# Kernel optimization log

Hardware: AMD Instinct MI355X
Metric: run time of the kernel (lower is better)

## Reference

```python
import jax, jax.numpy as jnp
import numpy as np

N_NODES = 50000


def _gcn_norm(edge_index, num_nodes):
    """PyG GCNConv normalization: add self-loops, symmetric deg^{-1/2} weights."""
    loops = jnp.arange(num_nodes, dtype=edge_index.dtype)
    src = jnp.concatenate([edge_index[0], loops])
    dst = jnp.concatenate([edge_index[1], loops])
    deg = jax.ops.segment_sum(jnp.ones_like(dst, dtype=jnp.float32), dst,
                              num_segments=num_nodes)
    dinv = jax.lax.rsqrt(jnp.maximum(deg, 1.0))  # self-loops guarantee deg>=1
    norm = dinv[src] * dinv[dst]                 # [E + N]
    return src, dst, norm


def _gcn_conv(x, W, b, src, dst, norm, num_nodes):
    h = x @ W                                    # [N, out] dense GEMM
    msg = h[src] * norm[:, None]                 # gather + scale
    agg = jax.ops.segment_sum(msg, dst, num_segments=num_nodes)
    return agg + b


def setup_inputs() -> dict:
    key = jax.random.key(0)
    ks = jax.random.split(key, 8)
    d = 128
    scale = 1.0 / np.sqrt(d)
    emb = jax.random.normal(ks[0], (N_NODES, d), dtype=jnp.float32)
    W1 = jax.random.normal(ks[1], (d, d), dtype=jnp.float32) * scale
    W2 = jax.random.normal(ks[2], (d, d), dtype=jnp.float32) * scale
    W3 = jax.random.normal(ks[3], (d, d), dtype=jnp.float32) * scale
    b1 = jnp.zeros((d,), dtype=jnp.float32)
    b2 = jnp.zeros((d,), dtype=jnp.float32)
    b3 = jnp.zeros((d,), dtype=jnp.float32)
    edge_index = jax.random.randint(ks[4], (2, 600000), 0, N_NODES, dtype=jnp.int64)
    return {"emb": emb, "W1": W1, "b1": b1, "W2": W2, "b2": b2,
            "W3": W3, "b3": b3, "edge_index": edge_index}


def reference(emb, W1, b1, W2, b2, W3, b3, edge_index):
    # Eval-mode forward: F.dropout(training=False) is identity.
    src, dst, norm = _gcn_norm(edge_index, N_NODES)
    x = emb
    x = jax.nn.relu(_gcn_conv(x, W1, b1, src, dst, norm, N_NODES))
    x = jax.nn.relu(_gcn_conv(x, W2, b2, src, dst, norm, N_NODES))
    x = _gcn_conv(x, W3, b3, src, dst, norm, N_NODES)
    x = x.at[0].set(0.0)  # x[0] = zeros(x.shape[1])
    return x
```

## Files before the change

### kernel.cpp

```cpp
#include <hip/hip_runtime.h>
#include <hip/hip_fp16.h>

#define NN 50000
#define D 128
#define STRIDE 64

typedef __attribute__((ext_vector_type(16))) float f32x16;
typedef _Float16 h16;
typedef __attribute__((ext_vector_type(8))) _Float16 h16x8;

struct alignas(16) H8 { h16 h[8]; };

typedef const __attribute__((address_space(1))) void gvoid;
typedef __attribute__((address_space(3))) void lvoid;

__global__ __launch_bounds__(256) void wprep_kernel(const float* __restrict__ W1,
                                                    const float* __restrict__ W2,
                                                    const float* __restrict__ W3,
                                                    h16* __restrict__ Wsp,
                                                    int* __restrict__ cnt) {
    const int b  = blockIdx.x;
    const int w  = b >> 3;
    const int ks = b & 7;
    const float* W = w == 0 ? W1 : (w == 1 ? W2 : W3);
    h16* dst = Wsp + w * 32768;
    const int l  = threadIdx.x & 63;
    const int ct = threadIdx.x >> 6;
    const int n  = ct * 32 + (l & 31);
    const int lh = l >> 5;
    const int kbase = ks * 16 + lh * 8;
    H8 hi8, lo8;
#pragma unroll
    for (int j = 0; j < 8; j++) {
        float wv = W[(kbase + j) * D + n];
        h16 hi = (h16)wv;
        hi8.h[j] = hi;
        lo8.h[j] = (h16)(wv - (float)hi);
    }
    const int base = ((ks * 4 + ct) * 64 + l) * 8;
    *(H8*)(dst + base)         = hi8;
    *(H8*)(dst + base + 16384) = lo8;
    for (int i = b * 256 + threadIdx.x; i < NN; i += 24 * 256) cnt[i] = 0;
}

__global__ __launch_bounds__(512, 4) void gemm_mfma(const void* __restrict__ Xv, int x_is_f32,
                                                    const h16* __restrict__ Wsp,
                                                    h16* __restrict__ H, int M,
                                                    const int* __restrict__ srcA,
                                                    const int* __restrict__ dstA,
                                                    int* __restrict__ cnt,
                                                    int* __restrict__ slots, int noct) {
    __shared__ h16 Ws[32768];
    {
        const int t = threadIdx.x;
#pragma unroll
        for (int i = 0; i < 8; i++) {
            const int off = (i * 512 + t) * 8;
            __builtin_amdgcn_global_load_lds((gvoid*)(Wsp + off), (lvoid*)(Ws + off),
                                             16, 0, 0);
        }
    }
    __syncthreads();

    const int wave = threadIdx.x >> 6;
    const int lane = threadIdx.x & 63;
    const int row0 = blockIdx.x * 256 + wave * 32;
    const int arow = min(row0 + (lane & 31), M - 1);
    const int koff = (lane >> 5) * 8;

    f32x16 acc[4] = {};

#pragma unroll
    for (int ks = 0; ks < 8; ks++) {
        h16x8 ahi, alo;
        if (x_is_f32) {
            const float* p = (const float*)Xv + (size_t)arow * D + koff + ks * 16;
            float4 fa = *(const float4*)p;
            float4 fb = *(const float4*)(p + 4);
            float f[8] = {fa.x, fa.y, fa.z, fa.w, fb.x, fb.y, fb.z, fb.w};
#pragma unroll
            for (int j = 0; j < 8; j++) {
                h16 hi = (h16)f[j];
                ahi[j] = hi;
                alo[j] = (h16)(f[j] - (float)hi);
            }
        } else {
            const h16* p = (const h16*)Xv + (size_t)arow * D + koff + ks * 16;
            ahi = *(const h16x8*)p;
        }
#pragma unroll
        for (int ct = 0; ct < 4; ct++) {
            const int base = ((ks * 4 + ct) * 64 + lane) * 8;
            h16x8 bhi = *(const h16x8*)(Ws + base);
            h16x8 blo = *(const h16x8*)(Ws + base + 16384);
            acc[ct] = __builtin_amdgcn_mfma_f32_32x32x16_f16(ahi, bhi, acc[ct], 0, 0, 0);
            acc[ct] = __builtin_amdgcn_mfma_f32_32x32x16_f16(ahi, blo, acc[ct], 0, 0, 0);
            if (x_is_f32)
                acc[ct] = __builtin_amdgcn_mfma_f32_32x32x16_f16(alo, bhi, acc[ct], 0, 0, 0);
        }
    }

    __syncthreads();
    {
        h16* C_lds = Ws;
        const int col0 = lane & 31;
        const int lr0  = 4 * (lane >> 5);
#pragma unroll
        for (int ct = 0; ct < 4; ct++) {
#pragma unroll
            for (int r = 0; r < 16; r++) {
                const int lrow = lr0 + (r & 3) + 8 * (r >> 2);
                C_lds[(wave * 32 + lrow) * D + ct * 32 + col0] = (h16)acc[ct][r];
            }
        }
        const h16* src = C_lds + wave * 32 * D;
        h16* gdst = H + (size_t)row0 * D;
#pragma unroll
        for (int j = 0; j < 8; j++) {
            const int i = j * 64 + lane;
            const int row = row0 + (i >> 4);
            if (row < M)
                *(h16x8*)(gdst + (size_t)i * 8) = *(const h16x8*)(src + i * 8);
        }
    }

    if (srcA) {
        int t = blockIdx.x * 512 + threadIdx.x;
        if (t < noct) {
            int4 sa = ((const int4*)srcA)[2 * t];
            int4 sb = ((const int4*)srcA)[2 * t + 1];
            int4 da = ((const int4*)dstA)[2 * t];
            int4 db = ((const int4*)dstA)[2 * t + 1];
            int p0 = atomicAdd(&cnt[da.x], 1);
            int p1 = atomicAdd(&cnt[da.y], 1);
            int p2 = atomicAdd(&cnt[da.z], 1);
            int p3 = atomicAdd(&cnt[da.w], 1);
            int p4 = atomicAdd(&cnt[db.x], 1);
            int p5 = atomicAdd(&cnt[db.y], 1);
            int p6 = atomicAdd(&cnt[db.z], 1);
            int p7 = atomicAdd(&cnt[db.w], 1);
            if (p0 < STRIDE - 4) slots[da.x * STRIDE + p0] = sa.x;
            if (p1 < STRIDE - 4) slots[da.y * STRIDE + p1] = sa.y;
            if (p2 < STRIDE - 4) slots[da.z * STRIDE + p2] = sa.z;
            if (p3 < STRIDE - 4) slots[da.w * STRIDE + p3] = sa.w;
            if (p4 < STRIDE - 4) slots[db.x * STRIDE + p4] = sb.x;
            if (p5 < STRIDE - 4) slots[db.y * STRIDE + p5] = sb.y;
            if (p6 < STRIDE - 4) slots[db.z * STRIDE + p6] = sb.z;
            if (p7 < STRIDE - 4) slots[db.w * STRIDE + p7] = sb.w;
        }
    }
}

__global__ __launch_bounds__(256) void agg_kernel(const h16* __restrict__ H,
                                                  const int* __restrict__ cnt,
                                                  const int* __restrict__ slots,
                                                  const float* __restrict__ bias,
                                                  h16* __restrict__ out16,
                                                  float* __restrict__ out32,
                                                  int mode) {
    const int lane  = threadIdx.x & 63;
    const int q     = lane >> 4;
    const int col   = (lane & 15) * 8;
    const int node0 = blockIdx.x * 16 + (threadIdx.x >> 6) * 4;

    const float4 bb0 = *(const float4*)(bias + col);
    const float4 bb1 = *(const float4*)(bias + col + 4);

    int cA[4], sa0[4], sb0[4];
#pragma unroll
    for (int nn = 0; nn < 4; nn++) {
        cA[nn]  = cnt[node0 + nn];
        sa0[nn] = slots[(node0 + nn) * STRIDE + q];
        sb0[nn] = slots[(node0 + nn) * STRIDE + 4 + q];
    }

#pragma unroll 1
    for (int nn = 0; nn < 4; nn++) {
        const int node = node0 + nn;
        const int c = __builtin_amdgcn_readfirstlane(cA[nn]);
        const float di = rsqrtf((float)c + 1.0f);
        const int sbase = node * STRIDE;
        const int pc = min((c + 8) & ~7, STRIDE);

        float aA[8] = {0.f, 0.f, 0.f, 0.f, 0.f, 0.f, 0.f, 0.f};
        float aB[8] = {0.f, 0.f, 0.f, 0.f, 0.f, 0.f, 0.f, 0.f};

        int sa = sa0[nn];
        int sb = sb0[nn];

        for (int p = 0; p < pc; p += 8) {
            int sa_n = slots[sbase + min(p + 8 + q, STRIDE - 1)];
            int sb_n = slots[sbase + min(p + 12 + q, STRIDE - 1)];
            const int ja = p + q;
            const int jb = p + 4 + q;
            const int ca = (ja < c) ? sa : node;
            const int cb = (jb < c) ? sb : node;
            float wa = (ja < c) ? rsqrtf((float)cnt[ca] + 1.0f) : ((ja == c) ? di : 0.f);
            float wb = (jb < c) ? rsqrtf((float)cnt[cb] + 1.0f) : ((jb == c) ? di : 0.f);
            h16x8 va = *(const h16x8*)(H + (size_t)ca * D + col);
            h16x8 vb = *(const h16x8*)(H + (size_t)cb * D + col);
#pragma unroll
            for (int j = 0; j < 8; j++) {
                aA[j] = fmaf(wa, (float)va[j], aA[j]);
                aB[j] = fmaf(wb, (float)vb[j], aB[j]);
            }
            sa = sa_n; sb = sb_n;
        }

#pragma unroll
        for (int j = 0; j < 8; j++) {
            float v = aA[j] + aB[j];
            v += __shfl_xor(v, 16, 64);
            v += __shfl_xor(v, 32, 64);
            aA[j] = v;
        }

        if (lane < 16) {
            float r[8];
            r[0] = fmaf(di, aA[0], bb0.x); r[1] = fmaf(di, aA[1], bb0.y);
            r[2] = fmaf(di, aA[2], bb0.z); r[3] = fmaf(di, aA[3], bb0.w);
            r[4] = fmaf(di, aA[4], bb1.x); r[5] = fmaf(di, aA[5], bb1.y);
            r[6] = fmaf(di, aA[6], bb1.z); r[7] = fmaf(di, aA[7], bb1.w);
            if (mode == 0) {
                h16x8 o;
#pragma unroll
                for (int j = 0; j < 8; j++) o[j] = (h16)fmaxf(r[j], 0.f);
                *(h16x8*)(out16 + (size_t)node * D + col) = o;
            } else {
                if (node == 0) {
#pragma unroll
                    for (int j = 0; j < 8; j++) r[j] = 0.f;
                }
                *(float4*)(out32 + (size_t)node * D + col)     = make_float4(r[0], r[1], r[2], r[3]);
                *(float4*)(out32 + (size_t)node * D + col + 4) = make_float4(r[4], r[5], r[6], r[7]);
            }
        }
    }
}


extern "C" void kernel_launch(void* const* d_in, const int* in_sizes, int n_in,
                              void* d_out, int out_size, void* d_ws, size_t ws_size,
                              hipStream_t stream) {
    const float* emb = (const float*)d_in[0];
    const float* W1  = (const float*)d_in[1];
    const float* b1  = (const float*)d_in[2];
    const float* W2  = (const float*)d_in[3];
    const float* b2  = (const float*)d_in[4];
    const float* W3  = (const float*)d_in[5];
    const float* b3  = (const float*)d_in[6];
    const int*   ei  = (const int*)d_in[7];

    const int E = in_sizes[7] / 2;
    const int* srcA = ei;
    const int* dstA = ei + E;
    float* out = (float*)d_out;

    char* ws = (char*)d_ws;
    size_t off = 0;
    auto alloc = [&](size_t bytes) -> void* {
        void* p = ws + off;
        off = (off + bytes + 255) & ~(size_t)255;
        return p;
    };
    h16* h      = (h16*)alloc((size_t)NN * D * 2);
    h16* x16    = (h16*)alloc((size_t)NN * D * 2);
    int* cnt    = (int*)alloc((size_t)NN * 4);
    int* slots  = (int*)alloc((size_t)NN * STRIDE * 4);
    h16* Wsp    = (h16*)alloc((size_t)3 * 32768 * 2);

    const int gemm_grid = (NN + 255) / 256;
    const int agg_grid  = NN / 16;
    const int noct = E / 8;

    wprep_kernel<<<24, 256, 0, stream>>>(W1, W2, W3, Wsp, cnt);
    gemm_mfma<<<gemm_grid, 512, 0, stream>>>(emb, 1, Wsp, h, NN,
                                             srcA, dstA, cnt, slots, noct);
    agg_kernel<<<agg_grid, 256, 0, stream>>>(h, cnt, slots, b1, x16, nullptr, 0);
    gemm_mfma<<<gemm_grid, 512, 0, stream>>>(x16, 0, Wsp + 32768, h, NN,
                                             nullptr, nullptr, nullptr, nullptr, 0);
    agg_kernel<<<agg_grid, 256, 0, stream>>>(h, cnt, slots, b2, x16, nullptr, 0);
    gemm_mfma<<<gemm_grid, 512, 0, stream>>>(x16, 0, Wsp + 65536, h, NN,
                                             nullptr, nullptr, nullptr, nullptr, 0);
    agg_kernel<<<agg_grid, 256, 0, stream>>>(h, cnt, slots, b3, nullptr, out, 1);
}
```

Before: 244.0 us.

## Fuse aggregation with next layer GEMM using 16x16 MFMA tiles

Layers 1 and 2 now run a single fused kernel. Each wave aggregates 16 nodes into LDS, applies bias and relu, then multiplies the tile by the next weight matrix using 16x16x32 MFMA with hi/lo weight splitting. This removes the separate GEMM launches and the global round-trip of the intermediate activations. The weight prep emits a new fragment layout for W2 and W3, and the edge loads in the first GEMM are hoisted before the barrier. The trade-off is that each fused wave reads weights from global or L2 rather than LDS, and aggregation occupancy may change.

```diff
diff --git a/kernel.cpp b/kernel.cpp
--- a/kernel.cpp
+++ b/kernel.cpp
@@ -6,6 +6,7 @@
 #define STRIDE 64
 
 typedef __attribute__((ext_vector_type(16))) float f32x16;
+typedef __attribute__((ext_vector_type(4)))  float f32x4;
 typedef _Float16 h16;
 typedef __attribute__((ext_vector_type(8))) _Float16 h16x8;
 
@@ -21,29 +22,47 @@
                                                     int* __restrict__ cnt) {
     const int b  = blockIdx.x;
     const int w  = b >> 3;
-    const int ks = b & 7;
     const float* W = w == 0 ? W1 : (w == 1 ? W2 : W3);
     h16* dst = Wsp + w * 32768;
     const int l  = threadIdx.x & 63;
     const int ct = threadIdx.x >> 6;
-    const int n  = ct * 32 + (l & 31);
-    const int lh = l >> 5;
-    const int kbase = ks * 16 + lh * 8;
-    H8 hi8, lo8;
-#pragma unroll
-    for (int j = 0; j < 8; j++) {
-        float wv = W[(kbase + j) * D + n];
-        h16 hi = (h16)wv;
-        hi8.h[j] = hi;
-        lo8.h[j] = (h16)(wv - (float)hi);
-    }
-    const int base = ((ks * 4 + ct) * 64 + l) * 8;
-    *(H8*)(dst + base)         = hi8;
-    *(H8*)(dst + base + 16384) = lo8;
+
+    if (w == 0) {
+        const int ks = b & 7;
+        const int n  = ct * 32 + (l & 31);
+        const int kbase = ks * 16 + (l >> 5) * 8;
+        H8 hi8, lo8;
+#pragma unroll
+        for (int j = 0; j < 8; j++) {
+            float wv = W[(kbase + j) * D + n];
+            h16 hi = (h16)wv;
+            hi8.h[j] = hi;
+            lo8.h[j] = (h16)(wv - (float)hi);
+        }
+        const int base = ((ks * 4 + ct) * 64 + l) * 8;
+        *(H8*)(dst + base)         = hi8;
+        *(H8*)(dst + base + 16384) = lo8;
+    } else {
+        const int f  = (b & 7) * 4 + ct;
+        const int ks = f >> 3, nt = f & 7;
+        const int kbase = ks * 32 + (l >> 4) * 8;
+        const int n = nt * 16 + (l & 15);
+        H8 hi8, lo8;
+#pragma unroll
+        for (int j = 0; j < 8; j++) {
+            float wv = W[(kbase + j) * D + n];
+            h16 hi = (h16)wv;
+            hi8.h[j] = hi;
+            lo8.h[j] = (h16)(wv - (float)hi);
+        }
+        const int base = (f * 64 + l) * 8;
+        *(H8*)(dst + base)         = hi8;
+        *(H8*)(dst + base + 16384) = lo8;
+    }
     for (int i = b * 256 + threadIdx.x; i < NN; i += 24 * 256) cnt[i] = 0;
 }
 
-__global__ __launch_bounds__(512, 4) void gemm_mfma(const void* __restrict__ Xv, int x_is_f32,
+__global__ __launch_bounds__(512, 4) void gemm_mfma(const void* __restrict__ Xv,
                                                     const h16* __restrict__ Wsp,
                                                     h16* __restrict__ H, int M,
                                                     const int* __restrict__ srcA,
@@ -60,6 +79,20 @@
                                              16, 0, 0);
         }
     }
+
+    int4 esa, esb, eda, edb;
+    bool do_fill = false;
+    {
+        int t = blockIdx.x * 512 + threadIdx.x;
+        if (t < noct) {
+            do_fill = true;
+            esa = ((const int4*)srcA)[2 * t];
+            esb = ((const int4*)srcA)[2 * t + 1];
+            eda = ((const int4*)dstA)[2 * t];
+            edb = ((const int4*)dstA)[2 * t + 1];
+        }
+    }
+
     __syncthreads();
 
     const int wave = threadIdx.x >> 6;
@@ -73,20 +106,15 @@
 #pragma unroll
     for (int ks = 0; ks < 8; ks++) {
         h16x8 ahi, alo;
-        if (x_is_f32) {
-            const float* p = (const float*)Xv + (size_t)arow * D + koff + ks * 16;
-            float4 fa = *(const float4*)p;
-            float4 fb = *(const float4*)(p + 4);
-            float f[8] = {fa.x, fa.y, fa.z, fa.w, fb.x, fb.y, fb.z, fb.w};
-#pragma unroll
-            for (int j = 0; j < 8; j++) {
-                h16 hi = (h16)f[j];
-                ahi[j] = hi;
-                alo[j] = (h16)(f[j] - (float)hi);
-            }
-        } else {
-            const h16* p = (const h16*)Xv + (size_t)arow * D + koff + ks * 16;
-            ahi = *(const h16x8*)p;
+        const float* p = (const float*)Xv + (size_t)arow * D + koff + ks * 16;
+        float4 fa = *(const float4*)p;
+        float4 fb = *(const float4*)(p + 4);
+        float f[8] = {fa.x, fa.y, fa.z, fa.w, fb.x, fb.y, fb.z, fb.w};
+#pragma unroll
+        for (int j = 0; j < 8; j++) {
+            h16 hi = (h16)f[j];
+            ahi[j] = hi;
+            alo[j] = (h16)(f[j] - (float)hi);
         }
 #pragma unroll
         for (int ct = 0; ct < 4; ct++) {
@@ -95,8 +123,7 @@
             h16x8 blo = *(const h16x8*)(Ws + base + 16384);
             acc[ct] = __builtin_amdgcn_mfma_f32_32x32x16_f16(ahi, bhi, acc[ct], 0, 0, 0);
             acc[ct] = __builtin_amdgcn_mfma_f32_32x32x16_f16(ahi, blo, acc[ct], 0, 0, 0);
-            if (x_is_f32)
-                acc[ct] = __builtin_amdgcn_mfma_f32_32x32x16_f16(alo, bhi, acc[ct], 0, 0, 0);
+            acc[ct] = __builtin_amdgcn_mfma_f32_32x32x16_f16(alo, bhi, acc[ct], 0, 0, 0);
         }
     }
 
@@ -124,29 +151,143 @@
         }
     }
 
-    if (srcA) {
-        int t = blockIdx.x * 512 + threadIdx.x;
-        if (t < noct) {
-            int4 sa = ((const int4*)srcA)[2 * t];
-            int4 sb = ((const int4*)srcA)[2 * t + 1];
-            int4 da = ((const int4*)dstA)[2 * t];
-            int4 db = ((const int4*)dstA)[2 * t + 1];
-            int p0 = atomicAdd(&cnt[da.x], 1);
-            int p1 = atomicAdd(&cnt[da.y], 1);
-            int p2 = atomicAdd(&cnt[da.z], 1);
-            int p3 = atomicAdd(&cnt[da.w], 1);
-            int p4 = atomicAdd(&cnt[db.x], 1);
-            int p5 = atomicAdd(&cnt[db.y], 1);
-            int p6 = atomicAdd(&cnt[db.z], 1);
-            int p7 = atomicAdd(&cnt[db.w], 1);
-            if (p0 < STRIDE - 4) slots[da.x * STRIDE + p0] = sa.x;
-            if (p1 < STRIDE - 4) slots[da.y * STRIDE + p1] = sa.y;
-            if (p2 < STRIDE - 4) slots[da.z * STRIDE + p2] = sa.z;
-            if (p3 < STRIDE - 4) slots[da.w * STRIDE + p3] = sa.w;
-            if (p4 < STRIDE - 4) slots[db.x * STRIDE + p4] = sb.x;
-            if (p5 < STRIDE - 4) slots[db.y * STRIDE + p5] = sb.y;
-            if (p6 < STRIDE - 4) slots[db.z * STRIDE + p6] = sb.z;
-            if (p7 < STRIDE - 4) slots[db.w * STRIDE + p7] = sb.w;
+    if (do_fill) {
+        int p0 = atomicAdd(&cnt[eda.x], 1);
+        int p1 = atomicAdd(&cnt[eda.y], 1);
+        int p2 = atomicAdd(&cnt[eda.z], 1);
+        int p3 = atomicAdd(&cnt[eda.w], 1);
+        int p4 = atomicAdd(&cnt[edb.x], 1);
+        int p5 = atomicAdd(&cnt[edb.y], 1);
+        int p6 = atomicAdd(&cnt[edb.z], 1);
+        int p7 = atomicAdd(&cnt[edb.w], 1);
+        if (p0 < STRIDE - 4) slots[eda.x * STRIDE + p0] = esa.x;
+        if (p1 < STRIDE - 4) slots[eda.y * STRIDE + p1] = esa.y;
+        if (p2 < STRIDE - 4) slots[eda.z * STRIDE + p2] = esa.z;
+        if (p3 < STRIDE - 4) slots[eda.w * STRIDE + p3] = esa.w;
+        if (p4 < STRIDE - 4) slots[edb.x * STRIDE + p4] = esb.x;
+        if (p5 < STRIDE - 4) slots[edb.y * STRIDE + p5] = esb.y;
+        if (p6 < STRIDE - 4) slots[edb.z * STRIDE + p6] = esb.z;
+        if (p7 < STRIDE - 4) slots[edb.w * STRIDE + p7] = esb.w;
+    }
+}
+
+__global__ __launch_bounds__(256) void fused_ag(const h16* __restrict__ Hin,
+                                                const int* __restrict__ cnt,
+                                                const int* __restrict__ slots,
+                                                const float* __restrict__ bias,
+                                                const h16* __restrict__ Wsp16,
+                                                h16* __restrict__ Hout) {
+    __shared__ h16 At[4 * 2048];
+    const int wave = threadIdx.x >> 6;
+    const int lane = threadIdx.x & 63;
+    const int q    = lane >> 4;
+    const int col  = (lane & 15) * 8;
+    const int nb   = (blockIdx.x * 4 + wave) * 16;
+    char* Aw = (char*)(At + wave * 2048);
+
+    const float4 bb0 = *(const float4*)(bias + col);
+    const float4 bb1 = *(const float4*)(bias + col + 4);
+
+    int node = min(nb, NN - 1);
+    int cCur = cnt[node];
+    int sa = slots[node * STRIDE + q];
+    int sb = slots[node * STRIDE + 4 + q];
+
+#pragma unroll 1
+    for (int n = 0; n < 16; n++) {
+        const int nodeN = min(nb + n + 1, NN - 1);
+        int cNxt = cnt[nodeN];
+        int saN = slots[nodeN * STRIDE + q];
+        int sbN = slots[nodeN * STRIDE + 4 + q];
+
+        const int c = __builtin_amdgcn_readfirstlane(cCur);
+        const float di = rsqrtf((float)c + 1.0f);
+        const int sbase = node * STRIDE;
+        const int pc = min((c + 8) & ~7, STRIDE);
+
+        float aA[8] = {0.f,0.f,0.f,0.f,0.f,0.f,0.f,0.f};
+        float aB[8] = {0.f,0.f,0.f,0.f,0.f,0.f,0.f,0.f};
+
+        for (int p = 0; p < pc; p += 8) {
+            int sa_n = slots[sbase + min(p + 8 + q, STRIDE - 1)];
+            int sb_n = slots[sbase + min(p + 12 + q, STRIDE - 1)];
+            const int ja = p + q;
+            const int jb = p + 4 + q;
+            const int ca = (ja < c) ? sa : node;
+            const int cb = (jb < c) ? sb : node;
+            float wa = (ja < c) ? rsqrtf((float)cnt[ca] + 1.0f) : ((ja == c) ? di : 0.f);
+            float wb = (jb < c) ? rsqrtf((float)cnt[cb] + 1.0f) : ((jb == c) ? di : 0.f);
+            h16x8 va = *(const h16x8*)(Hin + (size_t)ca * D + col);
+            h16x8 vb = *(const h16x8*)(Hin + (size_t)cb * D + col);
+#pragma unroll
+            for (int j = 0; j < 8; j++) {
+                aA[j] = fmaf(wa, (float)va[j], aA[j]);
+                aB[j] = fmaf(wb, (float)vb[j], aB[j]);
+            }
+            sa = sa_n; sb = sb_n;
+        }
+
+#pragma unroll
+        for (int j = 0; j < 8; j++) {
+            float v = aA[j] + aB[j];
+            v += __shfl_xor(v, 16, 64);
+            v += __shfl_xor(v, 32, 64);
+            aA[j] = v;
+        }
+
+        if (lane < 16) {
+            float r[8];
+            r[0] = fmaf(di, aA[0], bb0.x); r[1] = fmaf(di, aA[1], bb0.y);
+            r[2] = fmaf(di, aA[2], bb0.z); r[3] = fmaf(di, aA[3], bb0.w);
+            r[4] = fmaf(di, aA[4], bb1.x); r[5] = fmaf(di, aA[5], bb1.y);
+            r[6] = fmaf(di, aA[6], bb1.z); r[7] = fmaf(di, aA[7], bb1.w);
+            h16x8 o;
+#pragma unroll
+            for (int j = 0; j < 8; j++) o[j] = (h16)fmaxf(r[j], 0.f);
+            *(h16x8*)(Aw + n * 256 + ((lane << 4) ^ (n << 4))) = o;
+        }
+        node = nodeN; cCur = cNxt; sa = saN; sb = sbN;
+    }
+
+    h16x8 af[4];
+    {
+        const int r = lane & 15;
+#pragma unroll
+        for (int ks = 0; ks < 4; ks++)
+            af[ks] = *(const h16x8*)(Aw + r * 256 +
+                                     ((((ks * 4 + (lane >> 4)) << 4)) ^ (r << 4)));
+    }
+    f32x4 acc[8] = {};
+#pragma unroll
+    for (int nt = 0; nt < 8; nt++) {
+#pragma unroll
+        for (int ks = 0; ks < 4; ks++) {
+            const int fb = ((ks * 8 + nt) * 64 + lane) * 8;
+            h16x8 bhi = *(const h16x8*)(Wsp16 + fb);
+            h16x8 blo = *(const h16x8*)(Wsp16 + fb + 16384);
+            acc[nt] = __builtin_amdgcn_mfma_f32_16x16x32_f16(af[ks], bhi, acc[nt], 0, 0, 0);
+            acc[nt] = __builtin_amdgcn_mfma_f32_16x16x32_f16(af[ks], blo, acc[nt], 0, 0, 0);
+        }
+    }
+    {
+        const int crow0 = (lane >> 4) * 4;
+        const int cb = (lane & 15) * 2;
+#pragma unroll
+        for (int nt = 0; nt < 8; nt++) {
+#pragma unroll
+            for (int rg = 0; rg < 4; rg++) {
+                const int row = crow0 + rg;
+                *(h16*)(Aw + row * 256 + ((nt * 32 + cb) ^ (row << 4))) = (h16)acc[nt][rg];
+            }
+        }
+#pragma unroll
+        for (int j = 0; j < 4; j++) {
+            const int i = j * 64 + lane;
+            const int row = i >> 4, g = i & 15;
+            if (nb + row < NN) {
+                h16x8 v = *(const h16x8*)(Aw + row * 256 + ((g << 4) ^ (row << 4)));
+                *(h16x8*)(Hout + (size_t)(nb + row) * D + g * 8) = v;
+            }
         }
     }
 }
@@ -155,9 +296,7 @@
                                                   const int* __restrict__ cnt,
                                                   const int* __restrict__ slots,
                                                   const float* __restrict__ bias,
-                                                  h16* __restrict__ out16,
-                                                  float* __restrict__ out32,
-                                                  int mode) {
+                                                  float* __restrict__ out32) {
     const int lane  = threadIdx.x & 63;
     const int q     = lane >> 4;
     const int col   = (lane & 15) * 8;
@@ -182,8 +321,8 @@
         const int sbase = node * STRIDE;
         const int pc = min((c + 8) & ~7, STRIDE);
 
-        float aA[8] = {0.f, 0.f, 0.f, 0.f, 0.f, 0.f, 0.f, 0.f};
-        float aB[8] = {0.f, 0.f, 0.f, 0.f, 0.f, 0.f, 0.f, 0.f};
+        float aA[8] = {0.f,0.f,0.f,0.f,0.f,0.f,0.f,0.f};
+        float aB[8] = {0.f,0.f,0.f,0.f,0.f,0.f,0.f,0.f};
 
         int sa = sa0[nn];
         int sb = sb0[nn];
@@ -221,19 +360,12 @@
             r[2] = fmaf(di, aA[2], bb0.z); r[3] = fmaf(di, aA[3], bb0.w);
             r[4] = fmaf(di, aA[4], bb1.x); r[5] = fmaf(di, aA[5], bb1.y);
             r[6] = fmaf(di, aA[6], bb1.z); r[7] = fmaf(di, aA[7], bb1.w);
-            if (mode == 0) {
-                h16x8 o;
-#pragma unroll
-                for (int j = 0; j < 8; j++) o[j] = (h16)fmaxf(r[j], 0.f);
-                *(h16x8*)(out16 + (size_t)node * D + col) = o;
-            } else {
-                if (node == 0) {
-#pragma unroll
-                    for (int j = 0; j < 8; j++) r[j] = 0.f;
-                }
-                *(float4*)(out32 + (size_t)node * D + col)     = make_float4(r[0], r[1], r[2], r[3]);
-                *(float4*)(out32 + (size_t)node * D + col + 4) = make_float4(r[4], r[5], r[6], r[7]);
-            }
+            if (node == 0) {
+#pragma unroll
+                for (int j = 0; j < 8; j++) r[j] = 0.f;
+            }
+            *(float4*)(out32 + (size_t)node * D + col)     = make_float4(r[0], r[1], r[2], r[3]);
+            *(float4*)(out32 + (size_t)node * D + col + 4) = make_float4(r[4], r[5], r[6], r[7]);
         }
     }
 }
@@ -263,24 +395,21 @@
         off = (off + bytes + 255) & ~(size_t)255;
         return p;
     };
-    h16* h      = (h16*)alloc((size_t)NN * D * 2);
-    h16* x16    = (h16*)alloc((size_t)NN * D * 2);
+    h16* hA     = (h16*)alloc((size_t)NN * D * 2);
+    h16* hB     = (h16*)alloc((size_t)NN * D * 2);
     int* cnt    = (int*)alloc((size_t)NN * 4);
     int* slots  = (int*)alloc((size_t)NN * STRIDE * 4);
     h16* Wsp    = (h16*)alloc((size_t)3 * 32768 * 2);
 
-    const int gemm_grid = (NN + 255) / 256;
-    const int agg_grid  = NN / 16;
+    const int gemm_grid  = (NN + 255) / 256;
+    const int fused_grid = (NN + 63) / 64;
+    const int agg_grid   = NN / 16;
     const int noct = E / 8;
 
     wprep_kernel<<<24, 256, 0, stream>>>(W1, W2, W3, Wsp, cnt);
-    gemm_mfma<<<gemm_grid, 512, 0, stream>>>(emb, 1, Wsp, h, NN,
+    gemm_mfma<<<gemm_grid, 512, 0, stream>>>(emb, Wsp, hA, NN,
                                              srcA, dstA, cnt, slots, noct);
-    agg_kernel<<<agg_grid, 256, 0, stream>>>(h, cnt, slots, b1, x16, nullptr, 0);
-    gemm_mfma<<<gemm_grid, 512, 0, stream>>>(x16, 0, Wsp + 32768, h, NN,
-                                             nullptr, nullptr, nullptr, nullptr, 0);
-    agg_kernel<<<agg_grid, 256, 0, stream>>>(h, cnt, slots, b2, x16, nullptr, 0);
-    gemm_mfma<<<gemm_grid, 512, 0, stream>>>(x16, 0, Wsp + 65536, h, NN,
-                                             nullptr, nullptr, nullptr, nullptr, 0);
-    agg_kernel<<<agg_grid, 256, 0, stream>>>(h, cnt, slots, b3, nullptr, out, 1);
+    fused_ag<<<fused_grid, 256, 0, stream>>>(hA, cnt, slots, b1, Wsp + 32768, hB);
+    fused_ag<<<fused_grid, 256, 0, stream>>>(hB, cnt, slots, b2, Wsp + 65536, hA);
+    agg_kernel<<<agg_grid, 256, 0, stream>>>(hA, cnt, slots, b3, out);
 }
```

Result: slower. 259.7 us (+6.4%).
